# Kernel optimization log

Hardware: AMD Instinct MI355X
Metric: run time of the kernel (lower is better)

Reference implementation:

```python
import jax, jax.numpy as jnp
import numpy as np

N_NODES = 50000
N_EDGES = 800000
N_SUPPORTS = 3
F_IN = 128
F_OUT = 128
BATCH = 1


def _spmm(rows_k, cols_k, vals_k, sup, n_nodes):
    # sup: [B, N, F] dense features; sparse adj given as COO (rows, cols, vals)
    # out[b, r, :] += vals * sup[b, c, :]
    gathered = sup[:, cols_k, :] * vals_k[None, :, None]  # [B, E, F]
    seg = jax.vmap(lambda g: jax.ops.segment_sum(g, rows_k, num_segments=n_nodes))
    return seg(gathered)  # [B, N, F]


def setup_inputs() -> dict:
    key = jax.random.key(0)
    k1, k2, k3, k4, k5 = jax.random.split(key, 5)
    x = jax.random.normal(k1, (BATCH, N_NODES, F_IN), dtype=jnp.float32)
    rows = jax.random.randint(k2, (N_SUPPORTS, N_EDGES), 0, N_NODES)
    cols = jax.random.randint(k3, (N_SUPPORTS, N_EDGES), 0, N_NODES)
    vals = jax.random.uniform(k4, (N_SUPPORTS, N_EDGES), dtype=jnp.float32)
    kernels = jax.random.normal(k5, (N_SUPPORTS, F_IN, F_OUT), dtype=jnp.float32) * (2.0 / (F_IN + F_OUT)) ** 0.5
    bias = jnp.zeros((F_OUT,), dtype=jnp.float32)
    return {"x": x, "rows": rows, "cols": cols, "vals": vals, "kernels": kernels, "bias": bias}


def reference(x, rows, cols, vals, kernels, bias):
    n_nodes = x.shape[1]
    out = None
    for k in range(kernels.shape[0]):  # small fixed number of Chebyshev supports
        sup = jnp.einsum('bnf,fo->bno', x, kernels[k])  # dense feature transform
        acc = _spmm(rows[k], cols[k], vals[k], sup, n_nodes)
        out = acc if out is None else out + acc
    out = out + bias  # bias broadcast over [B, N, F_OUT]
    return jax.nn.relu(out)
```

## Files before the change

kernel.cpp:

```cpp
#include <hip/hip_runtime.h>

#define N_NODES 50000
#define N_EDGES 800000
#define N_SUP   3
#define FD      128
#define NP_PAD  50176

#define NB      196
#define RPB     256
#define EPB     3125
#define NBLK_E  256

typedef __attribute__((ext_vector_type(8))) short bf16x8;
typedef __attribute__((ext_vector_type(4))) float f32x4;

__device__ __forceinline__ unsigned rtn_bf16(float f) {
    unsigned u = __float_as_uint(f);
    return (u + 0x7FFFu + ((u >> 16) & 1u)) >> 16;
}
__device__ __forceinline__ float bf_lo(unsigned g) { return __uint_as_float(g << 16); }
__device__ __forceinline__ float bf_hi(unsigned g) { return __uint_as_float(g & 0xFFFF0000u); }

__global__ __launch_bounds__(256) void cvt_x_kernel(const float4* __restrict__ x4,
                                                    uint2* __restrict__ xb) {
    int i = blockIdx.x * 256 + threadIdx.x;
    if (i >= N_NODES * 32) return;
    float4 v = x4[i];
    xb[i] = make_uint2(rtn_bf16(v.x) | (rtn_bf16(v.y) << 16),
                       rtn_bf16(v.z) | (rtn_bf16(v.w) << 16));
}

__global__ __launch_bounds__(256) void cvt_w_kernel(const float* __restrict__ W,
                                                    uint4* __restrict__ wtb) {
    int tid = blockIdx.x * 256 + threadIdx.x;
    if (tid >= 128 * 48) return;
    int col = tid / 48, p = tid % 48;
    int qlog = (p & ~3) | ((p & 3) ^ ((col >> 1) & 3));
    int k0 = qlog * 8;
    unsigned w0 = rtn_bf16(W[(k0 + 0) * 128 + col]) | (rtn_bf16(W[(k0 + 1) * 128 + col]) << 16);
    unsigned w1 = rtn_bf16(W[(k0 + 2) * 128 + col]) | (rtn_bf16(W[(k0 + 3) * 128 + col]) << 16);
    unsigned w2 = rtn_bf16(W[(k0 + 4) * 128 + col]) | (rtn_bf16(W[(k0 + 5) * 128 + col]) << 16);
    unsigned w3 = rtn_bf16(W[(k0 + 6) * 128 + col]) | (rtn_bf16(W[(k0 + 7) * 128 + col]) << 16);
    wtb[col * 48 + p] = make_uint4(w0, w1, w2, w3);
}

__global__ __launch_bounds__(256) void bhist_kernel(const int* __restrict__ rows,
                                                    int* __restrict__ ghist) {
    __shared__ int hist[NB];
    int t = threadIdx.x, y = blockIdx.y, blk = blockIdx.x;
    for (int i = t; i < NB; i += 256) hist[i] = 0;
    __syncthreads();
    size_t ebase = (size_t)y * N_EDGES + (size_t)blk * EPB;
    for (int i = t; i < EPB; i += 256)
        atomicAdd(&hist[rows[ebase + i] >> 8], 1);
    __syncthreads();
    for (int i = t; i < NB; i += 256)
        if (hist[i]) atomicAdd(&ghist[y * NB + i], hist[i]);
}

__global__ __launch_bounds__(256) void bscan_kernel(const int* __restrict__ ghist,
                                                    int* __restrict__ bucket_start,
                                                    int* __restrict__ gcur) {
    __shared__ int s[256];
    int t = threadIdx.x, y = blockIdx.y;
    int cnt = (t < NB) ? ghist[y * NB + t] : 0;
    int val = cnt;
    s[t] = val; __syncthreads();
    for (int off = 1; off < 256; off <<= 1) {
        int v = (t >= off) ? s[t - off] : 0;
        __syncthreads();
        val += v; s[t] = val;
        __syncthreads();
    }
    int excl = val - cnt;
    if (t < NB) { bucket_start[y * (NB + 1) + t] = excl; gcur[y * NB + t] = excl; }
    if (t == NB - 1) bucket_start[y * (NB + 1) + NB] = val;
}

__global__ __launch_bounds__(256) void part_kernel(const int* __restrict__ rows,
                                                   const int* __restrict__ cols,
                                                   const float* __restrict__ vals,
                                                   int* __restrict__ gcur,
                                                   int4* __restrict__ tmp) {
    __shared__ int4     eS[EPB];
    __shared__ unsigned packed[EPB];
    __shared__ int hist[NB], lstart[NB], lcur[NB], gbase[NB];
    __shared__ int s[256];

    int t = threadIdx.x, y = blockIdx.y, blk = blockIdx.x;
    size_t ebase = (size_t)y * N_EDGES + (size_t)blk * EPB;

    for (int i = t; i < NB; i += 256) hist[i] = 0;
    __syncthreads();
    for (int i = t; i < EPB; i += 256) {
        int r = rows[ebase + i];
        int c = cols[ebase + i];
        float v = vals[ebase + i];
        eS[i] = make_int4(r, c, __float_as_int(v), 0);
        atomicAdd(&hist[r >> 8], 1);
    }
    __syncthreads();

    int cnt = (t < NB) ? hist[t] : 0;
    int val = cnt;
    s[t] = val; __syncthreads();
    for (int off = 1; off < 256; off <<= 1) {
        int v = (t >= off) ? s[t - off] : 0;
        __syncthreads();
        val += v; s[t] = val;
        __syncthreads();
    }
    if (t < NB) {
        int excl = val - cnt;
        lstart[t] = excl; lcur[t] = excl;
        if (cnt > 0) gbase[t] = atomicAdd(&gcur[y * NB + t], cnt);
    }
    __syncthreads();

    for (int i = t; i < EPB; i += 256) {
        int b = eS[i].x >> 8;
        int pos = atomicAdd(&lcur[b], 1);
        packed[pos] = ((unsigned)b << 16) | (unsigned)i;
    }
    __syncthreads();

    for (int i = t; i < EPB; i += 256) {
        unsigned p = packed[i];
        int b = p >> 16, idx = p & 0xFFFF;
        tmp[(size_t)y * N_EDGES + gbase[b] + (i - lstart[b])] = eS[idx];
    }
}

__global__ __launch_bounds__(256) void rowsort_kernel(const int4* __restrict__ tmp,
                                                      const int* __restrict__ bucket_start,
                                                      int2* __restrict__ payload,
                                                      int* __restrict__ row_start) {
    __shared__ int rhist[RPB], rcur[RPB];
    __shared__ int s[256];

    int t = threadIdx.x, b = blockIdx.x, y = blockIdx.y;
    int start = bucket_start[y * (NB + 1) + b];
    int end   = bucket_start[y * (NB + 1) + b + 1];
    int cnt   = end - start;

    rhist[t] = 0;
    __syncthreads();
    const int4* src = tmp + (size_t)y * N_EDGES + start;
    for (int i = t; i < cnt; i += 256)
        atomicAdd(&rhist[src[i].x & 255], 1);
    __syncthreads();

    int c0 = rhist[t];
    int val = c0;
    s[t] = val; __syncthreads();
    for (int off = 1; off < 256; off <<= 1) {
        int v = (t >= off) ? s[t - off] : 0;
        __syncthreads();
        val += v; s[t] = val;
        __syncthreads();
    }
    int excl = val - c0;
    rcur[t] = excl;
    int grow = b * RPB + t;
    if (grow < N_NODES) row_start[y * NP_PAD + grow] = start + excl;
    if (b == NB - 1 && t == 0) row_start[y * NP_PAD + N_NODES] = N_EDGES;
    __syncthreads();

    int2* dst = payload + (size_t)y * N_EDGES + start;
    for (int i = t; i < cnt; i += 256) {
        int4 e = src[i];
        int pos = atomicAdd(&rcur[e.x & 255], 1);
        dst[pos] = make_int2(e.y, e.z);
    }
}

__global__ __launch_bounds__(256) void gather_kernel(const unsigned* __restrict__ xb,
                                                     const int2* __restrict__ payload,
                                                     const int* __restrict__ row_start,
                                                     unsigned* __restrict__ zb) {
    int wid  = threadIdx.x >> 6;
    int lane = threadIdx.x & 63;
    int r = blockIdx.x * 4 + wid;
    if (r >= N_NODES) return;

    const int*  rs  = row_start + blockIdx.y * NP_PAD;
    const int2* pay = payload + (size_t)blockIdx.y * N_EDGES;
    int s = rs[r];
    int e = rs[r + 1];

    float2 a0 = {0.f, 0.f}, a1 = {0.f, 0.f}, a2 = {0.f, 0.f}, a3 = {0.f, 0.f};
    int i = s;
    for (; i + 8 <= e; i += 8) {
        int2 p0 = pay[i + 0], p1 = pay[i + 1], p2 = pay[i + 2], p3 = pay[i + 3];
        int2 p4 = pay[i + 4], p5 = pay[i + 5], p6 = pay[i + 6], p7 = pay[i + 7];
        unsigned g0 = xb[(size_t)p0.x * 64 + lane];
        unsigned g1 = xb[(size_t)p1.x * 64 + lane];
        unsigned g2 = xb[(size_t)p2.x * 64 + lane];
        unsigned g3 = xb[(size_t)p3.x * 64 + lane];
        unsigned g4 = xb[(size_t)p4.x * 64 + lane];
        unsigned g5 = xb[(size_t)p5.x * 64 + lane];
        unsigned g6 = xb[(size_t)p6.x * 64 + lane];
        unsigned g7 = xb[(size_t)p7.x * 64 + lane];
        float v0 = __int_as_float(p0.y), v1 = __int_as_float(p1.y);
        float v2 = __int_as_float(p2.y), v3 = __int_as_float(p3.y);
        float v4 = __int_as_float(p4.y), v5 = __int_as_float(p5.y);
        float v6 = __int_as_float(p6.y), v7 = __int_as_float(p7.y);
        a0.x = fmaf(v0, bf_lo(g0), a0.x); a0.y = fmaf(v0, bf_hi(g0), a0.y);
        a1.x = fmaf(v1, bf_lo(g1), a1.x); a1.y = fmaf(v1, bf_hi(g1), a1.y);
        a2.x = fmaf(v2, bf_lo(g2), a2.x); a2.y = fmaf(v2, bf_hi(g2), a2.y);
        a3.x = fmaf(v3, bf_lo(g3), a3.x); a3.y = fmaf(v3, bf_hi(g3), a3.y);
        a0.x = fmaf(v4, bf_lo(g4), a0.x); a0.y = fmaf(v4, bf_hi(g4), a0.y);
        a1.x = fmaf(v5, bf_lo(g5), a1.x); a1.y = fmaf(v5, bf_hi(g5), a1.y);
        a2.x = fmaf(v6, bf_lo(g6), a2.x); a2.y = fmaf(v6, bf_hi(g6), a2.y);
        a3.x = fmaf(v7, bf_lo(g7), a3.x); a3.y = fmaf(v7, bf_hi(g7), a3.y);
    }
    for (; i + 4 <= e; i += 4) {
        int2 p0 = pay[i + 0], p1 = pay[i + 1], p2 = pay[i + 2], p3 = pay[i + 3];
        unsigned g0 = xb[(size_t)p0.x * 64 + lane];
        unsigned g1 = xb[(size_t)p1.x * 64 + lane];
        unsigned g2 = xb[(size_t)p2.x * 64 + lane];
        unsigned g3 = xb[(size_t)p3.x * 64 + lane];
        float v0 = __int_as_float(p0.y), v1 = __int_as_float(p1.y);
        float v2 = __int_as_float(p2.y), v3 = __int_as_float(p3.y);
        a0.x = fmaf(v0, bf_lo(g0), a0.x); a0.y = fmaf(v0, bf_hi(g0), a0.y);
        a1.x = fmaf(v1, bf_lo(g1), a1.x); a1.y = fmaf(v1, bf_hi(g1), a1.y);
        a2.x = fmaf(v2, bf_lo(g2), a2.x); a2.y = fmaf(v2, bf_hi(g2), a2.y);
        a3.x = fmaf(v3, bf_lo(g3), a3.x); a3.y = fmaf(v3, bf_hi(g3), a3.y);
    }
    for (; i < e; ++i) {
        int2 p = pay[i];
        float v = __int_as_float(p.y);
        unsigned g = xb[(size_t)p.x * 64 + lane];
        a0.x = fmaf(v, bf_lo(g), a0.x); a0.y = fmaf(v, bf_hi(g), a0.y);
    }
    float ax = (a0.x + a1.x) + (a2.x + a3.x);
    float ay = (a0.y + a1.y) + (a2.y + a3.y);
    unsigned u = (blockIdx.y << 6) + lane;
    unsigned usw = u ^ (((unsigned)(r >> 1) & 3u) << 2);
    zb[(size_t)r * 192 + usw] = rtn_bf16(ax) | (rtn_bf16(ay) << 16);
}

__global__ __launch_bounds__(256) void mfma_gemm_kernel(const char* __restrict__ zb_sw,
                                                        const char* __restrict__ wtb_sw,
                                                        const float* __restrict__ bias,
                                                        float* __restrict__ out) {
    __shared__ __align__(16) char zS[2048];
    __shared__ __align__(16) char wS[8192];

    const int t    = threadIdx.x;
    const int lane = t & 63;
    const int wv   = t >> 6;
    const int row0 = blockIdx.x * 32;
    const int m = lane >> 4;
    const int n = lane & 15;

    const int ar0   = n;
    const int ar1   = 16 + n;
    const int aoff0 = ar0 * 64 + ((m ^ ((ar0 >> 1) & 3)) * 16);
    const int aoff1 = ar1 * 64 + ((m ^ ((ar1 >> 1) & 3)) * 16);
    const int col0  = wv * 32 + n;
    const int col1  = col0 + 16;
    const int boff0 = col0 * 64 + ((m ^ ((col0 >> 1) & 3)) * 16);
    const int boff1 = col1 * 64 + ((m ^ ((col1 >> 1) & 3)) * 16);

    f32x4 acc00 = {0.f, 0.f, 0.f, 0.f};
    f32x4 acc01 = acc00, acc10 = acc00, acc11 = acc00;

    for (int ks = 0; ks < 12; ++ks) {
        __syncthreads();
        if (t < 128) {
            const char* asrc = zb_sw + (size_t)(row0 + (t >> 2)) * 768 + ks * 64 + (t & 3) * 16;
            __builtin_amdgcn_global_load_lds(
                (const __attribute__((address_space(1))) void*)asrc,
                (__attribute__((address_space(3))) void*)(zS + t * 16), 16, 0, 0);
        }
        {
            const char* bsrc0 = wtb_sw + (t >> 2) * 768 + ks * 64 + (t & 3) * 16;
            __builtin_amdgcn_global_load_lds(
                (const __attribute__((address_space(1))) void*)bsrc0,
                (__attribute__((address_space(3))) void*)(wS + t * 16), 16, 0, 0);
            int i = t + 256;
            const char* bsrc1 = wtb_sw + (i >> 2) * 768 + ks * 64 + (i & 3) * 16;
            __builtin_amdgcn_global_load_lds(
                (const __attribute__((address_space(1))) void*)bsrc1,
                (__attribute__((address_space(3))) void*)(wS + i * 16), 16, 0, 0);
        }
        __syncthreads();

        bf16x8 a0 = *(const bf16x8*)(zS + aoff0);
        bf16x8 a1 = *(const bf16x8*)(zS + aoff1);
        bf16x8 b0 = *(const bf16x8*)(wS + boff0);
        bf16x8 b1 = *(const bf16x8*)(wS + boff1);
        acc00 = __builtin_amdgcn_mfma_f32_16x16x32_bf16(a0, b0, acc00, 0, 0, 0);
        acc01 = __builtin_amdgcn_mfma_f32_16x16x32_bf16(a0, b1, acc01, 0, 0, 0);
        acc10 = __builtin_amdgcn_mfma_f32_16x16x32_bf16(a1, b0, acc10, 0, 0, 0);
        acc11 = __builtin_amdgcn_mfma_f32_16x16x32_bf16(a1, b1, acc11, 0, 0, 0);
    }

    float bv0 = bias[col0], bv1 = bias[col1];
    #pragma unroll
    for (int j = 0; j < 4; ++j) {
        int r0 = row0 + m * 4 + j;
        int r1 = r0 + 16;
        if (r0 < N_NODES) {
            out[(size_t)r0 * 128 + col0] = fmaxf(acc00[j] + bv0, 0.f);
            out[(size_t)r0 * 128 + col1] = fmaxf(acc01[j] + bv1, 0.f);
        }
        if (r1 < N_NODES) {
            out[(size_t)r1 * 128 + col0] = fmaxf(acc10[j] + bv0, 0.f);
            out[(size_t)r1 * 128 + col1] = fmaxf(acc11[j] + bv1, 0.f);
        }
    }
}

extern "C" void kernel_launch(void* const* d_in, const int* in_sizes, int n_in,
                              void* d_out, int out_size, void* d_ws, size_t ws_size,
                              hipStream_t stream) {
    const float* x    = (const float*)d_in[0];
    const int*   rows = (const int*)d_in[1];
    const int*   cols = (const int*)d_in[2];
    const float* vals = (const float*)d_in[3];
    const float* kern = (const float*)d_in[4];
    const float* bias = (const float*)d_in[5];
    float* out = (float*)d_out;
    char* ws = (char*)d_ws;

    const size_t OFF_ZB  = 0;
    const size_t OFF_XB  = 38400000;
    const size_t OFF_PAY = OFF_XB + 12800000;
    const size_t OFF_RS  = OFF_PAY + (size_t)N_SUP * N_EDGES * 8;
    const size_t OFF_GH  = OFF_RS + (size_t)N_SUP * NP_PAD * 4;
    const size_t OFF_GC  = OFF_GH + 2368;
    const size_t OFF_BS  = OFF_GC + 2368;
    const size_t OFF_WT  = OFF_BS + 2368;

    unsigned* zb           = (unsigned*)(ws + OFF_ZB);
    int4*     tmp          = (int4*)    (ws + OFF_ZB);
    unsigned* xbuf         = (unsigned*)(ws + OFF_XB);
    int2*     payload      = (int2*)    (ws + OFF_PAY);
    int*      row_start    = (int*)     (ws + OFF_RS);
    int*      ghist        = (int*)     (ws + OFF_GH);
    int*      gcur         = (int*)     (ws + OFF_GC);
    int*      bucket_start = (int*)     (ws + OFF_BS);
    uint4*    wtb          = (uint4*)   (ws + OFF_WT);

    const int row_blocks  = (N_NODES + 3) / 4;
    const int gemm_blocks = (N_NODES + 31) / 32;

    hipMemsetAsync(ghist, 0, N_SUP * NB * 4, stream);
    cvt_x_kernel<<<(N_NODES * 32 + 255) / 256, 256, 0, stream>>>(
        (const float4*)x, (uint2*)xbuf);
    cvt_w_kernel<<<(128 * 48 + 255) / 256, 256, 0, stream>>>(kern, wtb);
    bhist_kernel<<<dim3(NBLK_E, N_SUP), 256, 0, stream>>>(rows, ghist);
    bscan_kernel<<<dim3(1, N_SUP), 256, 0, stream>>>(ghist, bucket_start, gcur);
    part_kernel<<<dim3(NBLK_E, N_SUP), 256, 0, stream>>>(rows, cols, vals, gcur, tmp);
    rowsort_kernel<<<dim3(NB, N_SUP), 256, 0, stream>>>(tmp, bucket_start,
                                                        payload, row_start);
    gather_kernel<<<dim3(row_blocks, N_SUP), 256, 0, stream>>>(
        xbuf, payload, row_start, zb);
    mfma_gemm_kernel<<<gemm_blocks, 256, 0, stream>>>(
        (const char*)zb, (const char*)wtb, bias, out);
}
```

Baseline: 282.2 us.

## Pack partition temp to 8-byte edges and vectorize gather with 16-byte row loads

The partition stage now packs the column index and the low row byte into one int, so each temp record is an int2 instead of an int4, which halves temp writes and reads in the partition and row-sort kernels. The gather kernel splits each wave into four 16-lane groups. Each group handles a different edge and loads 16 bytes of bf16 features per lane, and the four partial sums are combined with cross-lane shuffles before one group writes the swizzled 16-byte output. This reduces per-edge memory instructions and increases the number of edges in flight, at the cost of the shuffle reductions and the assumption that column indices fit in 16 bits.

```diff
diff --git a/kernel.cpp b/kernel.cpp
--- a/kernel.cpp
+++ b/kernel.cpp
@@ -81,9 +81,10 @@
                                                    const int* __restrict__ cols,
                                                    const float* __restrict__ vals,
                                                    int* __restrict__ gcur,
-                                                   int4* __restrict__ tmp) {
-    __shared__ int4     eS[EPB];
-    __shared__ unsigned packed[EPB];
+                                                   int2* __restrict__ tmp) {
+    __shared__ int2          eS[EPB];
+    __shared__ unsigned      packed[EPB];
+    __shared__ unsigned char bS[EPB];
     __shared__ int hist[NB], lstart[NB], lcur[NB], gbase[NB];
     __shared__ int s[256];
 
@@ -96,7 +97,8 @@
         int r = rows[ebase + i];
         int c = cols[ebase + i];
         float v = vals[ebase + i];
-        eS[i] = make_int4(r, c, __float_as_int(v), 0);
+        eS[i] = make_int2(c | ((r & 255) << 16), __float_as_int(v));
+        bS[i] = (unsigned char)(r >> 8);
         atomicAdd(&hist[r >> 8], 1);
     }
     __syncthreads();
@@ -118,7 +120,7 @@
     __syncthreads();
 
     for (int i = t; i < EPB; i += 256) {
-        int b = eS[i].x >> 8;
+        int b = bS[i];
         int pos = atomicAdd(&lcur[b], 1);
         packed[pos] = ((unsigned)b << 16) | (unsigned)i;
     }
@@ -131,7 +133,7 @@
     }
 }
 
-__global__ __launch_bounds__(256) void rowsort_kernel(const int4* __restrict__ tmp,
+__global__ __launch_bounds__(256) void rowsort_kernel(const int2* __restrict__ tmp,
                                                       const int* __restrict__ bucket_start,
                                                       int2* __restrict__ payload,
                                                       int* __restrict__ row_start) {
@@ -145,9 +147,9 @@
 
     rhist[t] = 0;
     __syncthreads();
-    const int4* src = tmp + (size_t)y * N_EDGES + start;
+    const int2* src = tmp + (size_t)y * N_EDGES + start;
     for (int i = t; i < cnt; i += 256)
-        atomicAdd(&rhist[src[i].x & 255], 1);
+        atomicAdd(&rhist[((unsigned)src[i].x) >> 16], 1);
     __syncthreads();
 
     int c0 = rhist[t];
@@ -168,18 +170,20 @@
 
     int2* dst = payload + (size_t)y * N_EDGES + start;
     for (int i = t; i < cnt; i += 256) {
-        int4 e = src[i];
-        int pos = atomicAdd(&rcur[e.x & 255], 1);
-        dst[pos] = make_int2(e.y, e.z);
-    }
-}
-
-__global__ __launch_bounds__(256) void gather_kernel(const unsigned* __restrict__ xb,
+        int2 e = src[i];
+        int pos = atomicAdd(&rcur[((unsigned)e.x) >> 16], 1);
+        dst[pos] = make_int2(e.x & 0xFFFF, e.y);
+    }
+}
+
+__global__ __launch_bounds__(256) void gather_kernel(const uint4* __restrict__ xb4,
                                                      const int2* __restrict__ payload,
                                                      const int* __restrict__ row_start,
-                                                     unsigned* __restrict__ zb) {
+                                                     uint4* __restrict__ zb4) {
     int wid  = threadIdx.x >> 6;
     int lane = threadIdx.x & 63;
+    int grp  = lane >> 4;
+    int l16  = lane & 15;
     int r = blockIdx.x * 4 + wid;
     if (r >= N_NODES) return;
 
@@ -188,56 +192,83 @@
     int s = rs[r];
     int e = rs[r + 1];
 
-    float2 a0 = {0.f, 0.f}, a1 = {0.f, 0.f}, a2 = {0.f, 0.f}, a3 = {0.f, 0.f};
+    float a0 = 0.f, a1 = 0.f, a2 = 0.f, a3 = 0.f;
+    float a4 = 0.f, a5 = 0.f, a6 = 0.f, a7 = 0.f;
+
     int i = s;
+    for (; i + 16 <= e; i += 16) {
+        int2 pA = pay[i + grp];
+        int2 pB = pay[i + 4 + grp];
+        int2 pC = pay[i + 8 + grp];
+        int2 pD = pay[i + 12 + grp];
+        uint4 gA = xb4[(size_t)pA.x * 16 + l16];
+        uint4 gB = xb4[(size_t)pB.x * 16 + l16];
+        uint4 gC = xb4[(size_t)pC.x * 16 + l16];
+        uint4 gD = xb4[(size_t)pD.x * 16 + l16];
+        float vA = __int_as_float(pA.y), vB = __int_as_float(pB.y);
+        float vC = __int_as_float(pC.y), vD = __int_as_float(pD.y);
+        a0 = fmaf(vA, bf_lo(gA.x), a0); a1 = fmaf(vA, bf_hi(gA.x), a1);
+        a2 = fmaf(vA, bf_lo(gA.y), a2); a3 = fmaf(vA, bf_hi(gA.y), a3);
+        a4 = fmaf(vA, bf_lo(gA.z), a4); a5 = fmaf(vA, bf_hi(gA.z), a5);
+        a6 = fmaf(vA, bf_lo(gA.w), a6); a7 = fmaf(vA, bf_hi(gA.w), a7);
+        a0 = fmaf(vB, bf_lo(gB.x), a0); a1 = fmaf(vB, bf_hi(gB.x), a1);
+        a2 = fmaf(vB, bf_lo(gB.y), a2); a3 = fmaf(vB, bf_hi(gB.y), a3);
+        a4 = fmaf(vB, bf_lo(gB.z), a4); a5 = fmaf(vB, bf_hi(gB.z), a5);
+        a6 = fmaf(vB, bf_lo(gB.w), a6); a7 = fmaf(vB, bf_hi(gB.w), a7);
+        a0 = fmaf(vC, bf_lo(gC.x), a0); a1 = fmaf(vC, bf_hi(gC.x), a1);
+        a2 = fmaf(vC, bf_lo(gC.y), a2); a3 = fmaf(vC, bf_hi(gC.y), a3);
+        a4 = fmaf(vC, bf_lo(gC.z), a4); a5 = fmaf(vC, bf_hi(gC.z), a5);
+        a6 = fmaf(vC, bf_lo(gC.w), a6); a7 = fmaf(vC, bf_hi(gC.w), a7);
+        a0 = fmaf(vD, bf_lo(gD.x), a0); a1 = fmaf(vD, bf_hi(gD.x), a1);
+        a2 = fmaf(vD, bf_lo(gD.y), a2); a3 = fmaf(vD, bf_hi(gD.y), a3);
+        a4 = fmaf(vD, bf_lo(gD.z), a4); a5 = fmaf(vD, bf_hi(gD.z), a5);
+        a6 = fmaf(vD, bf_lo(gD.w), a6); a7 = fmaf(vD, bf_hi(gD.w), a7);
+    }
     for (; i + 8 <= e; i += 8) {
-        int2 p0 = pay[i + 0], p1 = pay[i + 1], p2 = pay[i + 2], p3 = pay[i + 3];
-        int2 p4 = pay[i + 4], p5 = pay[i + 5], p6 = pay[i + 6], p7 = pay[i + 7];
-        unsigned g0 = xb[(size_t)p0.x * 64 + lane];
-        unsigned g1 = xb[(size_t)p1.x * 64 + lane];
-        unsigned g2 = xb[(size_t)p2.x * 64 + lane];
-        unsigned g3 = xb[(size_t)p3.x * 64 + lane];
-        unsigned g4 = xb[(size_t)p4.x * 64 + lane];
-        unsigned g5 = xb[(size_t)p5.x * 64 + lane];
-        unsigned g6 = xb[(size_t)p6.x * 64 + lane];
-        unsigned g7 = xb[(size_t)p7.x * 64 + lane];
-        float v0 = __int_as_float(p0.y), v1 = __int_as_float(p1.y);
-        float v2 = __int_as_float(p2.y), v3 = __int_as_float(p3.y);
-        float v4 = __int_as_float(p4.y), v5 = __int_as_float(p5.y);
-        float v6 = __int_as_float(p6.y), v7 = __int_as_float(p7.y);
-        a0.x = fmaf(v0, bf_lo(g0), a0.x); a0.y = fmaf(v0, bf_hi(g0), a0.y);
-        a1.x = fmaf(v1, bf_lo(g1), a1.x); a1.y = fmaf(v1, bf_hi(g1), a1.y);
-        a2.x = fmaf(v2, bf_lo(g2), a2.x); a2.y = fmaf(v2, bf_hi(g2), a2.y);
-        a3.x = fmaf(v3, bf_lo(g3), a3.x); a3.y = fmaf(v3, bf_hi(g3), a3.y);
-        a0.x = fmaf(v4, bf_lo(g4), a0.x); a0.y = fmaf(v4, bf_hi(g4), a0.y);
-        a1.x = fmaf(v5, bf_lo(g5), a1.x); a1.y = fmaf(v5, bf_hi(g5), a1.y);
-        a2.x = fmaf(v6, bf_lo(g6), a2.x); a2.y = fmaf(v6, bf_hi(g6), a2.y);
-        a3.x = fmaf(v7, bf_lo(g7), a3.x); a3.y = fmaf(v7, bf_hi(g7), a3.y);
-    }
-    for (; i + 4 <= e; i += 4) {
-        int2 p0 = pay[i + 0], p1 = pay[i + 1], p2 = pay[i + 2], p3 = pay[i + 3];
-        unsigned g0 = xb[(size_t)p0.x * 64 + lane];
-        unsigned g1 = xb[(size_t)p1.x * 64 + lane];
-        unsigned g2 = xb[(size_t)p2.x * 64 + lane];
-        unsigned g3 = xb[(size_t)p3.x * 64 + lane];
-        float v0 = __int_as_float(p0.y), v1 = __int_as_float(p1.y);
-        float v2 = __int_as_float(p2.y), v3 = __int_as_float(p3.y);
-        a0.x = fmaf(v0, bf_lo(g0), a0.x); a0.y = fmaf(v0, bf_hi(g0), a0.y);
-        a1.x = fmaf(v1, bf_lo(g1), a1.x); a1.y = fmaf(v1, bf_hi(g1), a1.y);
-        a2.x = fmaf(v2, bf_lo(g2), a2.x); a2.y = fmaf(v2, bf_hi(g2), a2.y);
-        a3.x = fmaf(v3, bf_lo(g3), a3.x); a3.y = fmaf(v3, bf_hi(g3), a3.y);
-    }
-    for (; i < e; ++i) {
-        int2 p = pay[i];
-        float v = __int_as_float(p.y);
-        unsigned g = xb[(size_t)p.x * 64 + lane];
-        a0.x = fmaf(v, bf_lo(g), a0.x); a0.y = fmaf(v, bf_hi(g), a0.y);
-    }
-    float ax = (a0.x + a1.x) + (a2.x + a3.x);
-    float ay = (a0.y + a1.y) + (a2.y + a3.y);
-    unsigned u = (blockIdx.y << 6) + lane;
-    unsigned usw = u ^ (((unsigned)(r >> 1) & 3u) << 2);
-    zb[(size_t)r * 192 + usw] = rtn_bf16(ax) | (rtn_bf16(ay) << 16);
+        int2 pA = pay[i + grp];
+        int2 pB = pay[i + 4 + grp];
+        uint4 gA = xb4[(size_t)pA.x * 16 + l16];
+        uint4 gB = xb4[(size_t)pB.x * 16 + l16];
+        float vA = __int_as_float(pA.y), vB = __int_as_float(pB.y);
+        a0 = fmaf(vA, bf_lo(gA.x), a0); a1 = fmaf(vA, bf_hi(gA.x), a1);
+        a2 = fmaf(vA, bf_lo(gA.y), a2); a3 = fmaf(vA, bf_hi(gA.y), a3);
+        a4 = fmaf(vA, bf_lo(gA.z), a4); a5 = fmaf(vA, bf_hi(gA.z), a5);
+        a6 = fmaf(vA, bf_lo(gA.w), a6); a7 = fmaf(vA, bf_hi(gA.w), a7);
+        a0 = fmaf(vB, bf_lo(gB.x), a0); a1 = fmaf(vB, bf_hi(gB.x), a1);
+        a2 = fmaf(vB, bf_lo(gB.y), a2); a3 = fmaf(vB, bf_hi(gB.y), a3);
+        a4 = fmaf(vB, bf_lo(gB.z), a4); a5 = fmaf(vB, bf_hi(gB.z), a5);
+        a6 = fmaf(vB, bf_lo(gB.w), a6); a7 = fmaf(vB, bf_hi(gB.w), a7);
+    }
+    for (; i < e; i += 4) {
+        int idx = i + grp;
+        if (idx < e) {
+            int2 p = pay[idx];
+            uint4 g = xb4[(size_t)p.x * 16 + l16];
+            float v = __int_as_float(p.y);
+            a0 = fmaf(v, bf_lo(g.x), a0); a1 = fmaf(v, bf_hi(g.x), a1);
+            a2 = fmaf(v, bf_lo(g.y), a2); a3 = fmaf(v, bf_hi(g.y), a3);
+            a4 = fmaf(v, bf_lo(g.z), a4); a5 = fmaf(v, bf_hi(g.z), a5);
+            a6 = fmaf(v, bf_lo(g.w), a6); a7 = fmaf(v, bf_hi(g.w), a7);
+        }
+    }
+
+    a0 += __shfl_xor(a0, 16); a0 += __shfl_xor(a0, 32);
+    a1 += __shfl_xor(a1, 16); a1 += __shfl_xor(a1, 32);
+    a2 += __shfl_xor(a2, 16); a2 += __shfl_xor(a2, 32);
+    a3 += __shfl_xor(a3, 16); a3 += __shfl_xor(a3, 32);
+    a4 += __shfl_xor(a4, 16); a4 += __shfl_xor(a4, 32);
+    a5 += __shfl_xor(a5, 16); a5 += __shfl_xor(a5, 32);
+    a6 += __shfl_xor(a6, 16); a6 += __shfl_xor(a6, 32);
+    a7 += __shfl_xor(a7, 16); a7 += __shfl_xor(a7, 32);
+
+    if (grp == 0) {
+        unsigned q = ((unsigned)(r >> 1)) & 3u;
+        uint4 o = make_uint4(rtn_bf16(a0) | (rtn_bf16(a1) << 16),
+                             rtn_bf16(a2) | (rtn_bf16(a3) << 16),
+                             rtn_bf16(a4) | (rtn_bf16(a5) << 16),
+                             rtn_bf16(a6) | (rtn_bf16(a7) << 16));
+        zb4[(size_t)r * 48 + blockIdx.y * 16 + (l16 ^ q)] = o;
+    }
 }
 
 __global__ __launch_bounds__(256) void mfma_gemm_kernel(const char* __restrict__ zb_sw,
@@ -335,7 +366,7 @@
     const size_t OFF_WT  = OFF_BS + 2368;
 
     unsigned* zb           = (unsigned*)(ws + OFF_ZB);
-    int4*     tmp          = (int4*)    (ws + OFF_ZB);
+    int2*     tmp          = (int2*)    (ws + OFF_ZB);
     unsigned* xbuf         = (unsigned*)(ws + OFF_XB);
     int2*     payload      = (int2*)    (ws + OFF_PAY);
     int*      row_start    = (int*)     (ws + OFF_RS);
@@ -357,7 +388,7 @@
     rowsort_kernel<<<dim3(NB, N_SUP), 256, 0, stream>>>(tmp, bucket_start,
                                                         payload, row_start);
     gather_kernel<<<dim3(row_blocks, N_SUP), 256, 0, stream>>>(
-        xbuf, payload, row_start, zb);
+        (const uint4*)xbuf, payload, row_start, (uint4*)zb);
     mfma_gemm_kernel<<<gemm_blocks, 256, 0, stream>>>(
         (const char*)zb, (const char*)wtb, bias, out);
 }
```

After: 255.4 us. 9.5% less time.
